# Kernel optimization log

Hardware: AMD Instinct MI355X
Metric: run time of the kernel (lower is better)

Reference implementation:

```python
import jax, jax.numpy as jnp
import numpy as np

HIDDEN = 4096
N_HEADS = 32
N_KV_HEADS = 8
HEAD_DIM = HIDDEN // N_HEADS  # 128
GROUPS = N_HEADS // N_KV_HEADS  # 4
B, S = 1, 2048
NEG = -1e9


def setup_inputs() -> dict:
    key = jax.random.key(0)
    ks = jax.random.split(key, 8)
    hidden_states = jax.random.normal(ks[0], (B, S, HIDDEN), dtype=jnp.float32)
    # additive causal mask [B,1,S,S]
    causal = jnp.tril(jnp.ones((S, S), dtype=bool))
    attention_mask = jnp.where(causal, 0.0, NEG).astype(jnp.float32)[None, None]
    position_ids = jnp.broadcast_to(jnp.arange(S, dtype=jnp.int64), (B, S))
    inv_freq = 1.0 / (500000.0 ** (np.arange(0, HEAD_DIM, 2, dtype=np.float32) / HEAD_DIM))
    freqs = np.arange(S, dtype=np.float32)[:, None] * inv_freq[None, :]  # [S, 64]
    cos = jnp.asarray(np.cos(freqs), dtype=jnp.float32)
    sin = jnp.asarray(np.sin(freqs), dtype=jnp.float32)
    sc = 1.0 / np.sqrt(HIDDEN)
    Wq = jax.random.normal(ks[1], (HIDDEN, HIDDEN), dtype=jnp.float32) * sc
    Wk = jax.random.normal(ks[2], (N_KV_HEADS * HEAD_DIM, HIDDEN), dtype=jnp.float32) * sc
    Wv = jax.random.normal(ks[3], (N_KV_HEADS * HEAD_DIM, HIDDEN), dtype=jnp.float32) * sc
    Wo = jax.random.normal(ks[4], (HIDDEN, HIDDEN), dtype=jnp.float32) * sc
    return {"hidden_states": hidden_states, "attention_mask": attention_mask,
            "position_ids": position_ids, "cos": cos, "sin": sin,
            "Wq": Wq, "Wk": Wk, "Wv": Wv, "Wo": Wo}


def _rope(q, k, cos, sin, position_ids):
    # cos/sin: [max_pos, head_dim//2]; gather per position -> [b,1,s,hd/2]
    c = cos[position_ids][:, None]  # [b,1,s,d/2]
    s_ = sin[position_ids][:, None]
    q1, q2 = q[..., ::2], q[..., 1::2]
    k1, k2 = k[..., ::2], k[..., 1::2]
    q_rot = jnp.concatenate([q1 * c - q2 * s_, q2 * c + q1 * s_], axis=-1)
    k_rot = jnp.concatenate([k1 * c - k2 * s_, k2 * c + k1 * s_], axis=-1)
    return q_rot, k_rot


def reference(hidden_states, attention_mask, position_ids, cos, sin, Wq, Wk, Wv, Wo):
    b, s, _ = hidden_states.shape
    q = jnp.einsum('bsh,oh->bso', hidden_states, Wq).reshape(b, s, N_HEADS, HEAD_DIM).transpose(0, 2, 1, 3)
    k = jnp.einsum('bsh,oh->bso', hidden_states, Wk).reshape(b, s, N_KV_HEADS, HEAD_DIM).transpose(0, 2, 1, 3)
    v = jnp.einsum('bsh,oh->bso', hidden_states, Wv).reshape(b, s, N_KV_HEADS, HEAD_DIM).transpose(0, 2, 1, 3)
    q, k = _rope(q, k, cos, sin, position_ids)
    if GROUPS > 1:
        k = jnp.repeat(k, GROUPS, axis=1)  # [b,H,s,d]
        v = jnp.repeat(v, GROUPS, axis=1)
    scores = jnp.einsum('bhqd,bhkd->bhqk', q, k) / np.sqrt(HEAD_DIM)
    scores = scores + attention_mask
    attn = jax.nn.softmax(scores.astype(jnp.float32), axis=-1).astype(q.dtype)
    out = jnp.einsum('bhqk,bhkd->bhqd', attn, v)
    out = out.transpose(0, 2, 1, 3).reshape(b, s, HIDDEN)
    out = jnp.einsum('bso,ho->bsh', out, Wo)
    return out
```

## Files before the change

### kernel.cpp

```cpp
#include <hip/hip_runtime.h>
#include <hip/hip_bf16.h>

#define S_LEN 2048
#define HID   4096
#define NH    32
#define NKV   8
#define HD    128

typedef __attribute__((ext_vector_type(8))) short short8v;
typedef __attribute__((ext_vector_type(4))) float floatx4;

__device__ __forceinline__ float bf2f(unsigned short u) {
  union { unsigned int u32; float f; } v; v.u32 = ((unsigned int)u) << 16; return v.f;
}
__device__ __forceinline__ unsigned short f2bf(float f) {
  union { float f; unsigned int u; } v; v.f = f;
  unsigned int u = v.u + 0x7fffu + ((v.u >> 16) & 1u);
  return (unsigned short)(u >> 16);
}

__device__ __forceinline__ void gld_lds16(const void* g, void* l) {
  __builtin_amdgcn_global_load_lds((const __attribute__((address_space(1))) void*)g,
                                   (__attribute__((address_space(3))) void*)l, 16, 0, 0);
}

__global__ __launch_bounds__(256) void cvt_all(const float* __restrict__ X,  const float* __restrict__ Wq,
                                               const float* __restrict__ Wk, const float* __restrict__ Wv,
                                               const float* __restrict__ Wo,
                                               unsigned short* __restrict__ Xb,  unsigned short* __restrict__ Wqb,
                                               unsigned short* __restrict__ Wkb, unsigned short* __restrict__ Wvb,
                                               unsigned short* __restrict__ Wob) {
  const int c0 = 2097152;
  const int c1 = c0 + 4194304;
  const int c2 = c1 + 1048576;
  const int c3 = c2 + 1048576;
  const int c4 = c3 + 4194304;
  int i = blockIdx.x * blockDim.x + threadIdx.x;
  int stride = gridDim.x * blockDim.x;
  for (; i < c4; i += stride) {
    const float* src; unsigned short* dst; int off;
    if (i < c0)      { src = X;  dst = Xb;  off = i; }
    else if (i < c1) { src = Wq; dst = Wqb; off = i - c0; }
    else if (i < c2) { src = Wk; dst = Wkb; off = i - c1; }
    else if (i < c3) { src = Wv; dst = Wvb; off = i - c2; }
    else             { src = Wo; dst = Wob; off = i - c3; }
    float4 v = ((const float4*)src)[off];
    ushort4 o;
    o.x = f2bf(v.x); o.y = f2bf(v.y); o.z = f2bf(v.z); o.w = f2bf(v.w);
    ((ushort4*)dst)[off] = o;
  }
}

__device__ __forceinline__ void gemm256_core(const unsigned short* __restrict__ A,
                                             const unsigned short* __restrict__ B,
                                             unsigned short* lds,
                                             int brow, int bcol, int tid,
                                             floatx4 acc[8][4]) {
  const int K = 4096;
  const int w = tid >> 6, lane = tid & 63;
  const int fr = lane & 15, fq = lane >> 4;
  const int wm = w >> 2, wn = w & 3;

  const int r0s = w * 32 + (lane >> 2);
  const int r1s = r0s + 16;
  const int sl0 = ((lane & 3) ^ ((r0s >> 1) & 3)) << 3;
  const int sl1 = ((lane & 3) ^ ((r1s >> 1) & 3)) << 3;
  const unsigned short* pAs0 = A + (size_t)(brow + r0s) * K + sl0;
  const unsigned short* pAs1 = A + (size_t)(brow + r1s) * K + sl1;
  const unsigned short* pBs0 = B + (size_t)(bcol + r0s) * K + sl0;
  const unsigned short* pBs1 = B + (size_t)(bcol + r1s) * K + sl1;

  const int sl = (fq ^ ((fr >> 1) & 3)) << 3;
  int aoffb[8], boffb[4];
#pragma unroll
  for (int m = 0; m < 8; ++m) aoffb[m] = (wm * 128 + m * 16 + fr) * 32 + sl;
#pragma unroll
  for (int n = 0; n < 4; ++n) boffb[n] = 16384 + (wn * 64 + n * 16 + fr) * 32 + sl;

#define STG_A(buf, kh, t)                                                     \
  do {                                                                        \
    const int ko_ = (t) * 64 + (kh) * 32;                                     \
    gld_lds16(pAs0 + ko_, lds + (buf) * 32768 + (kh) * 8192 + w * 1024);      \
    gld_lds16(pAs1 + ko_, lds + (buf) * 32768 + (kh) * 8192 + w * 1024 + 512);\
  } while (0)
#define STG_B(buf, kh, t)                                                     \
  do {                                                                        \
    const int ko_ = (t) * 64 + (kh) * 32;                                     \
    gld_lds16(pBs0 + ko_, lds + (buf) * 32768 + 16384 + (kh) * 8192 + w * 1024);      \
    gld_lds16(pBs1 + ko_, lds + (buf) * 32768 + 16384 + (kh) * 8192 + w * 1024 + 512);\
  } while (0)

  STG_A(0, 0, 0); STG_B(0, 0, 0);
  STG_A(0, 1, 0); STG_B(0, 1, 0);
  STG_A(1, 0, 1); STG_B(1, 0, 1);
  asm volatile("s_waitcnt vmcnt(8)" ::: "memory");
  __builtin_amdgcn_s_barrier();

  const int NT = K / 64;
  for (int t = 0; t < NT; ++t) {
    const int c = t & 1;
    const unsigned short* Lc = lds + c * 32768;
    short8v a_[4], b_[4], a2_[4];

#pragma unroll
    for (int m = 0; m < 4; ++m) a_[m] = *(const short8v*)&Lc[aoffb[m]];
#pragma unroll
    for (int n = 0; n < 4; ++n) b_[n] = *(const short8v*)&Lc[boffb[n]];
    if (t + 1 < NT) STG_A(c ^ 1, 1, t + 1);
    __builtin_amdgcn_s_setprio(1);
#pragma unroll
    for (int m = 0; m < 4; ++m)
#pragma unroll
      for (int n = 0; n < 4; ++n)
        acc[m][n] = __builtin_amdgcn_mfma_f32_16x16x32_bf16(a_[m], b_[n], acc[m][n], 0, 0, 0);
    __builtin_amdgcn_s_setprio(0);
    __builtin_amdgcn_s_barrier();

#pragma unroll
    for (int m = 0; m < 4; ++m) a2_[m] = *(const short8v*)&Lc[aoffb[m + 4]];
    if (t + 1 < NT) STG_B(c ^ 1, 1, t + 1);
    __builtin_amdgcn_s_setprio(1);
#pragma unroll
    for (int m = 0; m < 4; ++m)
#pragma unroll
      for (int n = 0; n < 4; ++n)
        acc[m + 4][n] = __builtin_amdgcn_mfma_f32_16x16x32_bf16(a2_[m], b_[n], acc[m + 4][n], 0, 0, 0);
    __builtin_amdgcn_s_setprio(0);
    if (t == NT - 1) asm volatile("s_waitcnt vmcnt(0)" ::: "memory");
    else             asm volatile("s_waitcnt vmcnt(8)" ::: "memory");
    __builtin_amdgcn_s_barrier();

#pragma unroll
    for (int m = 0; m < 4; ++m) a_[m] = *(const short8v*)&Lc[8192 + aoffb[m]];
#pragma unroll
    for (int n = 0; n < 4; ++n) b_[n] = *(const short8v*)&Lc[8192 + boffb[n]];
    if (t + 2 < NT) STG_A(c, 0, t + 2);
    __builtin_amdgcn_s_setprio(1);
#pragma unroll
    for (int m = 0; m < 4; ++m)
#pragma unroll
      for (int n = 0; n < 4; ++n)
        acc[m][n] = __builtin_amdgcn_mfma_f32_16x16x32_bf16(a_[m], b_[n], acc[m][n], 0, 0, 0);
    __builtin_amdgcn_s_setprio(0);
    __builtin_amdgcn_s_barrier();

#pragma unroll
    for (int m = 0; m < 4; ++m) a2_[m] = *(const short8v*)&Lc[8192 + aoffb[m + 4]];
    if (t + 2 < NT) STG_B(c, 0, t + 2);
    __builtin_amdgcn_s_setprio(1);
#pragma unroll
    for (int m = 0; m < 4; ++m)
#pragma unroll
      for (int n = 0; n < 4; ++n)
        acc[m + 4][n] = __builtin_amdgcn_mfma_f32_16x16x32_bf16(a2_[m], b_[n], acc[m + 4][n], 0, 0, 0);
    __builtin_amdgcn_s_setprio(0);
    if (t >= NT - 2) asm volatile("s_waitcnt vmcnt(0)" ::: "memory");
    else             asm volatile("s_waitcnt vmcnt(8)" ::: "memory");
    __builtin_amdgcn_s_barrier();
  }
#undef STG_A
#undef STG_B
}

__global__ __launch_bounds__(512, 2) void gemm_qkv(const unsigned short* __restrict__ Xb,
                                                   const unsigned short* __restrict__ Wqb,
                                                   const unsigned short* __restrict__ Wkb,
                                                   const unsigned short* __restrict__ Wvb,
                                                   unsigned short* __restrict__ Qg,
                                                   unsigned short* __restrict__ Kg,
                                                   unsigned short* __restrict__ Vt) {
  __shared__ unsigned short lds[2 * 32768];
  const int bx = blockIdx.x;
  const unsigned short* B; unsigned short* C; int mode, bcol, ldc;
  if (bx < 16)      { B = Wqb; C = Qg; mode = 0; bcol = bx * 256;        ldc = HID;  }
  else if (bx < 20) { B = Wkb; C = Kg; mode = 0; bcol = (bx - 16) * 256; ldc = 1024; }
  else              { B = Wvb; C = Vt; mode = 1; bcol = (bx - 20) * 256; ldc = 0;    }
  const int brow = blockIdx.y * 256;
  const int tid = threadIdx.x;
  floatx4 acc[8][4] = {};
  gemm256_core(Xb, B, lds, brow, bcol, tid, acc);

  const int w = tid >> 6, lane = tid & 63;
  const int fr = lane & 15, fq = lane >> 4;
  const int wm = w >> 2, wn = w & 3;
  const int r0 = brow + wm * 128 + fq * 4;
  const int c0 = bcol + wn * 64 + fr;
  if (mode == 0) {
#pragma unroll
    for (int m = 0; m < 8; ++m)
#pragma unroll
      for (int n = 0; n < 4; ++n)
#pragma unroll
        for (int r = 0; r < 4; ++r)
          C[(size_t)(r0 + m * 16 + r) * ldc + c0 + n * 16] = f2bf(acc[m][n][r]);
  } else {
#pragma unroll
    for (int m = 0; m < 8; ++m)
#pragma unroll
      for (int n = 0; n < 4; ++n) {
        ushort4 pk;
        pk.x = f2bf(acc[m][n][0]); pk.y = f2bf(acc[m][n][1]);
        pk.z = f2bf(acc[m][n][2]); pk.w = f2bf(acc[m][n][3]);
        *(ushort4*)&Vt[(size_t)(c0 + n * 16) * S_LEN + (r0 + m * 16)] = pk;
      }
  }
}

__device__ __forceinline__ void gemm_pipe_core(const unsigned short* __restrict__ A,
                                               const unsigned short* __restrict__ B,
                                               unsigned short* lds,
                                               int brow, int bcol, int tid,
                                               floatx4 acc[4][4]) {
  const int K = 4096;
  const int w = tid >> 6, lane = tid & 63;
  const int fr = lane & 15, fq = lane >> 4;
  const int wm = w >> 1, wn = w & 1;

  const int rA0 = tid >> 2, sA = tid & 3;
  const unsigned short* pA0 = A + (size_t)(brow + rA0) * K       + ((sA ^ (rA0 & 3)) << 3);
  const unsigned short* pA1 = A + (size_t)(brow + 128 + rA0) * K + ((sA ^ (rA0 & 3)) << 3);
  const unsigned short* pB0 = B + (size_t)(bcol + rA0) * K       + ((sA ^ (rA0 & 3)) << 3);

  const int sl = (fq ^ (fr & 3)) << 3;
  int aoff[4], boff[4];
#pragma unroll
  for (int m = 0; m < 4; ++m) aoff[m] = (wm * 64 + m * 16 + fr) * 32 + sl;
#pragma unroll
  for (int n = 0; n < 4; ++n) boff[n] = 8192 + (wn * 64 + n * 16 + fr) * 32 + sl;

#define STAGEG(buf, kofs)                                        \
  do {                                                           \
    unsigned short* b_ = lds + (buf) * 12288 + w * 512;          \
    gld_lds16(pA0 + (kofs), b_);                                 \
    gld_lds16(pA1 + (kofs), b_ + 4096);                          \
    gld_lds16(pB0 + (kofs), b_ + 8192);                          \
  } while (0)

  STAGEG(0, 0);
  STAGEG(1, 32);
  asm volatile("s_waitcnt vmcnt(3)" ::: "memory");
  __syncthreads();

  int cb = 0, nb = 2;
  for (int t = 0; t < 128; ++t) {
    if (t + 2 < 128) STAGEG(nb, (t + 2) * 32);

    const unsigned short* Lc = lds + cb * 12288;
    short8v a[4], b[4];
#pragma unroll
    for (int m = 0; m < 4; ++m) a[m] = *(const short8v*)&Lc[aoff[m]];
#pragma unroll
    for (int n = 0; n < 4; ++n) b[n] = *(const short8v*)&Lc[boff[n]];

    __builtin_amdgcn_s_setprio(1);
#pragma unroll
    for (int m = 0; m < 4; ++m)
#pragma unroll
      for (int n = 0; n < 4; ++n)
        acc[m][n] = __builtin_amdgcn_mfma_f32_16x16x32_bf16(a[m], b[n], acc[m][n], 0, 0, 0);
    __builtin_amdgcn_s_setprio(0);

    if (t + 1 < 128) {
      if (t + 2 < 128) asm volatile("s_waitcnt vmcnt(3)" ::: "memory");
      else             asm volatile("s_waitcnt vmcnt(0)" ::: "memory");
      __syncthreads();
      cb = (cb == 2) ? 0 : cb + 1;
      nb = (nb == 2) ? 0 : nb + 1;
    }
  }
#undef STAGEG
}

__global__ __launch_bounds__(512, 4) void gemm_o(const unsigned short* __restrict__ Ao,
                                                 const unsigned short* __restrict__ Wob,
                                                 float* __restrict__ Out) {
  __shared__ unsigned short lds[3 * 12288];
  const int tid = threadIdx.x;
  const int brow = blockIdx.y * 256, bcol = blockIdx.x * 128;
  floatx4 acc[4][4] = {};
  gemm_pipe_core(Ao, Wob, lds, brow, bcol, tid, acc);
  const int w = tid >> 6, lane = tid & 63;
  const int fr = lane & 15, fq = lane >> 4;
  const int r0 = brow + (w >> 1) * 64 + fq * 4;
  const int c0 = bcol + (w & 1) * 64 + fr;
#pragma unroll
  for (int m = 0; m < 4; ++m)
#pragma unroll
    for (int n = 0; n < 4; ++n)
#pragma unroll
      for (int r = 0; r < 4; ++r)
        Out[(size_t)(r0 + m * 16 + r) * HID + c0 + n * 16] = acc[m][n][r];
}

__global__ __launch_bounds__(256) void rope_kernel(const unsigned short* __restrict__ In,
                                                   const float* __restrict__ cosT,
                                                   const float* __restrict__ sinT,
                                                   unsigned short* __restrict__ Out,
                                                   int nh, float scale) {
  int idx = blockIdx.x * 256 + threadIdx.x;
  int j = idx & 63;
  int s = (idx >> 6) & (S_LEN - 1);
  int h = idx >> 17;
  unsigned int pr = *(const unsigned int*)(In + (size_t)s * (nh * HD) + h * HD + 2 * j);
  float q1 = bf2f((unsigned short)(pr & 0xffffu));
  float q2 = bf2f((unsigned short)(pr >> 16));
  float c = cosT[s * 64 + j], sn = sinT[s * 64 + j];
  unsigned short* op = Out + ((size_t)h * S_LEN + s) * HD + j;
  op[0]  = f2bf(scale * (q1 * c - q2 * sn));
  op[64] = f2bf(scale * (q2 * c + q1 * sn));
}

__global__ __launch_bounds__(256) void attn_fwd(const unsigned short* __restrict__ Qr,
                                                const unsigned short* __restrict__ Kr,
                                                const unsigned short* __restrict__ Vt,
                                                unsigned short* __restrict__ Ao) {
  __shared__ unsigned short Kl[2][64 * 128];
  __shared__ unsigned short Vl[2][64 * 128];
  __shared__ unsigned short Pl[4][16 * 72];
  const int id = blockIdx.x;
  const int swz = (id & 7) * 128 + (id >> 3);
  const int h  = swz >> 5;
  const int qt = 31 - (swz & 31);
  const int hk = h >> 2;
  const int qb = qt * 64;
  const int tid = threadIdx.x, w = tid >> 6, lane = tid & 63;
  const int fr = lane & 15, fq = lane >> 4;

  short8v aq[4];
  {
    const unsigned short* qp = Qr + ((size_t)(h * S_LEN + qb + w * 16 + fr)) * HD + fq * 8;
#pragma unroll
    for (int ks = 0; ks < 4; ++ks) aq[ks] = *(const short8v*)(qp + ks * 32);
  }

  const int kcb = ((tid & 15) * 16) ^ (((tid >> 4) & 7) << 4);
  const unsigned short* pK0 = Kr + ((size_t)hk * S_LEN + (tid >> 4)) * HD + (kcb >> 1);
  const int vcb = ((tid & 7) * 16) ^ (((tid >> 3) & 7) << 4);
  const unsigned short* pV0 = Vt + ((size_t)hk * HD + (tid >> 3)) * S_LEN + (vcb >> 1);

  float l_r[4] = {0.f, 0.f, 0.f, 0.f};
  floatx4 o[8] = {};

#define STAGE(buf, t)                                                          \
  do {                                                                         \
    const unsigned short* pk_ = pK0 + (size_t)(t) * 64 * HD;                   \
    const unsigned short* pv_ = pV0 + (t) * 64;                                \
    _Pragma("unroll")                                                          \
    for (int j = 0; j < 4; ++j)                                                \
      gld_lds16(pk_ + (size_t)j * 16 * HD, &Kl[buf][w * 512 + j * 2048]);      \
    _Pragma("unroll")                                                          \
    for (int j = 0; j < 4; ++j)                                                \
      gld_lds16(pv_ + (size_t)j * 32 * S_LEN, &Vl[buf][w * 512 + j * 2048]);   \
  } while (0)

  STAGE(0, 0);
  asm volatile("s_waitcnt vmcnt(0)" ::: "memory");
  __syncthreads();

  int cur = 0;
  for (int t = 0; t <= qt; ++t) {
    const int kv0 = t * 64;
    if (t < qt) STAGE(cur ^ 1, t + 1);

    floatx4 s4[4] = {};
    const unsigned short* Kc = &Kl[cur][0];
    const unsigned short* Vc = &Vl[cur][0];
    __builtin_amdgcn_s_setprio(1);
#pragma unroll
    for (int ks = 0; ks < 4; ++ks) {
#pragma unroll
      for (int n = 0; n < 4; ++n) {
        int row = n * 16 + fr;
        int cb = (ks * 64 + fq * 16) ^ ((row & 7) << 4);
        short8v bk = *(const short8v*)&Kc[row * 128 + (cb >> 1)];
        s4[n] = __builtin_amdgcn_mfma_f32_16x16x32_bf16(aq[ks], bk, s4[n], 0, 0, 0);
      }
    }
    __builtin_amdgcn_s_setprio(0);

    if (t == qt) {
#pragma unroll
      for (int n = 0; n < 4; ++n) {
        int col = kv0 + n * 16 + fr;
#pragma unroll
        for (int r = 0; r < 4; ++r) {
          int rowq = qb + w * 16 + fq * 4 + r;
          if (col > rowq) s4[n][r] = -1e30f;
        }
      }
    }

    float psum[4] = {0.f, 0.f, 0.f, 0.f};
#pragma unroll
    for (int n = 0; n < 4; ++n)
#pragma unroll
      for (int r = 0; r < 4; ++r) {
        float p = exp2f(s4[n][r]);
        psum[r] += p;
        Pl[w][(fq * 4 + r) * 72 + n * 16 + fr] = f2bf(p);
      }
#pragma unroll
    for (int r = 0; r < 4; ++r) l_r[r] += psum[r];

    short8v pa[2];
#pragma unroll
    for (int ks = 0; ks < 2; ++ks)
      pa[ks] = *(const short8v*)&Pl[w][fr * 72 + ks * 32 + fq * 8];
    __builtin_amdgcn_s_setprio(1);
#pragma unroll
    for (int nf = 0; nf < 8; ++nf) {
#pragma unroll
      for (int ks = 0; ks < 2; ++ks) {
        int row = nf * 16 + fr;
        int cb = (ks * 64 + fq * 16) ^ ((row & 7) << 4);
        short8v bv = *(const short8v*)&Vc[row * 64 + (cb >> 1)];
        o[nf] = __builtin_amdgcn_mfma_f32_16x16x32_bf16(pa[ks], bv, o[nf], 0, 0, 0);
      }
    }
    __builtin_amdgcn_s_setprio(0);

    if (t < qt) {
      asm volatile("s_waitcnt vmcnt(0)" ::: "memory");
      __syncthreads();
      cur ^= 1;
    }
  }
#undef STAGE

  float lsum[4];
#pragma unroll
  for (int r = 0; r < 4; ++r) lsum[r] = l_r[r];
#pragma unroll
  for (int off = 8; off; off >>= 1)
#pragma unroll
    for (int r = 0; r < 4; ++r) lsum[r] += __shfl_xor(lsum[r], off);
  float rinv[4];
#pragma unroll
  for (int r = 0; r < 4; ++r) rinv[r] = 1.0f / lsum[r];

  unsigned short* aop = Ao + (size_t)(qb + w * 16 + fq * 4) * HID + h * HD + fr;
#pragma unroll
  for (int nf = 0; nf < 8; ++nf)
#pragma unroll
    for (int r = 0; r < 4; ++r)
      aop[(size_t)r * HID + nf * 16] = f2bf(o[nf][r] * rinv[r]);
}

extern "C" void kernel_launch(void* const* d_in, const int* in_sizes, int n_in,
                              void* d_out, int out_size, void* d_ws, size_t ws_size,
                              hipStream_t stream) {
  (void)in_sizes; (void)n_in; (void)out_size; (void)ws_size;
  const float* X    = (const float*)d_in[0];
  const float* cosT = (const float*)d_in[3];
  const float* sinT = (const float*)d_in[4];
  const float* Wq   = (const float*)d_in[5];
  const float* Wk   = (const float*)d_in[6];
  const float* Wv   = (const float*)d_in[7];
  const float* Wo   = (const float*)d_in[8];

  char* ws = (char*)d_ws;
  size_t off = 0;
  auto alloc = [&](size_t bytes) { char* p = ws + off; off += (bytes + 255) & ~(size_t)255; return p; };
  unsigned short* Xb  = (unsigned short*)alloc((size_t)S_LEN * HID * 2);
  unsigned short* Wqb = (unsigned short*)alloc((size_t)HID * HID * 2);
  unsigned short* Wkb = (unsigned short*)alloc((size_t)1024 * HID * 2);
  unsigned short* Wvb = (unsigned short*)alloc((size_t)1024 * HID * 2);
  unsigned short* Wob = (unsigned short*)alloc((size_t)HID * HID * 2);
  unsigned short* Qg  = (unsigned short*)alloc((size_t)S_LEN * HID * 2);
  unsigned short* Kg  = (unsigned short*)alloc((size_t)S_LEN * 1024 * 2);
  unsigned short* Vt  = (unsigned short*)alloc((size_t)1024 * S_LEN * 2);
  unsigned short* Qr = Wqb;
  unsigned short* Kr = Wqb + (size_t)NH * S_LEN * HD;
  unsigned short* Ao = Xb;

  cvt_all<<<2048, 256, 0, stream>>>(X, Wq, Wk, Wv, Wo, Xb, Wqb, Wkb, Wvb, Wob);
  gemm_qkv<<<dim3(24, 8), 512, 0, stream>>>(Xb, Wqb, Wkb, Wvb, Qg, Kg, Vt);
  rope_kernel<<<(NH * S_LEN * 64) / 256, 256, 0, stream>>>(Qg, cosT, sinT, Qr, NH, 0.12751744f);
  rope_kernel<<<(NKV * S_LEN * 64) / 256, 256, 0, stream>>>(Kg, cosT, sinT, Kr, NKV, 1.0f);
  attn_fwd<<<1024, 256, 0, stream>>>(Qr, Kr, Vt, Ao);
  gemm_o<<<dim3(32, 8), 512, 0, stream>>>(Ao, Wob, (float*)d_out);
}
```

Baseline: 337.4 us.

## Restructure output GEMM pipeline and keep attention P in registers via shuffles

The output-projection GEMM is inlined into its kernel and now loads K-tiles of 64 in two halves, double-buffered with finer-grained vmcnt waits and raw s_barrier. Its LDS swizzle changes and occupancy drops to 2 blocks per CU. The attention kernel computes S transposed (K as the A operand) and packs P to bf16 with v_cvt_pk_bf16_f32. It then builds the PV A-operand with cross-lane shuffles instead of a round trip through LDS, and simplifies the row-sum reduction. The aim is less LDS traffic and fewer barriers, paid for with extra shuffle instructions and lower GEMM occupancy.

```diff
diff --git a/kernel.cpp b/kernel.cpp
--- a/kernel.cpp
+++ b/kernel.cpp
@@ -17,6 +17,11 @@
   union { float f; unsigned int u; } v; v.f = f;
   unsigned int u = v.u + 0x7fffu + ((v.u >> 16) & 1u);
   return (unsigned short)(u >> 16);
+}
+__device__ __forceinline__ unsigned int cvtpk_bf16(float lo, float hi) {
+  unsigned int r;
+  asm("v_cvt_pk_bf16_f32 %0, %1, %2" : "=v"(r) : "v"(lo), "v"(hi));
+  return r;
 }
 
 __device__ __forceinline__ void gld_lds16(const void* g, void* l) {
@@ -206,83 +211,89 @@
   }
 }
 
-__device__ __forceinline__ void gemm_pipe_core(const unsigned short* __restrict__ A,
-                                               const unsigned short* __restrict__ B,
-                                               unsigned short* lds,
-                                               int brow, int bcol, int tid,
-                                               floatx4 acc[4][4]) {
+__global__ __launch_bounds__(512, 2) void gemm_o(const unsigned short* __restrict__ Ao,
+                                                 const unsigned short* __restrict__ Wob,
+                                                 float* __restrict__ Out) {
+  __shared__ unsigned short lds[2 * 24576];
   const int K = 4096;
+  const int tid = threadIdx.x;
   const int w = tid >> 6, lane = tid & 63;
   const int fr = lane & 15, fq = lane >> 4;
   const int wm = w >> 1, wn = w & 1;
-
-  const int rA0 = tid >> 2, sA = tid & 3;
-  const unsigned short* pA0 = A + (size_t)(brow + rA0) * K       + ((sA ^ (rA0 & 3)) << 3);
-  const unsigned short* pA1 = A + (size_t)(brow + 128 + rA0) * K + ((sA ^ (rA0 & 3)) << 3);
-  const unsigned short* pB0 = B + (size_t)(bcol + rA0) * K       + ((sA ^ (rA0 & 3)) << 3);
-
-  const int sl = (fq ^ (fr & 3)) << 3;
+  const int brow = blockIdx.y * 256, bcol = blockIdx.x * 128;
+
+  const int rA = tid >> 2;
+  const int sA = ((tid & 3) ^ ((rA >> 1) & 3)) << 3;
+  const unsigned short* pA0 = Ao  + (size_t)(brow + rA) * K + sA;
+  const unsigned short* pA1 = Ao  + (size_t)(brow + 128 + rA) * K + sA;
+  const unsigned short* pB0 = Wob + (size_t)(bcol + rA) * K + sA;
+
+  const int sl = (fq ^ ((fr >> 1) & 3)) << 3;
   int aoff[4], boff[4];
 #pragma unroll
   for (int m = 0; m < 4; ++m) aoff[m] = (wm * 64 + m * 16 + fr) * 32 + sl;
 #pragma unroll
-  for (int n = 0; n < 4; ++n) boff[n] = 8192 + (wn * 64 + n * 16 + fr) * 32 + sl;
-
-#define STAGEG(buf, kofs)                                        \
-  do {                                                           \
-    unsigned short* b_ = lds + (buf) * 12288 + w * 512;          \
-    gld_lds16(pA0 + (kofs), b_);                                 \
-    gld_lds16(pA1 + (kofs), b_ + 4096);                          \
-    gld_lds16(pB0 + (kofs), b_ + 8192);                          \
+  for (int n = 0; n < 4; ++n) boff[n] = 16384 + (wn * 64 + n * 16 + fr) * 32 + sl;
+
+  floatx4 acc[4][4] = {};
+
+#define STG_KH(buf, kh, t)                                                       \
+  do {                                                                           \
+    const int ko_ = (t) * 64 + (kh) * 32;                                        \
+    gld_lds16(pA0 + ko_, lds + (buf) * 24576 + (kh) * 8192 + w * 512);           \
+    gld_lds16(pA1 + ko_, lds + (buf) * 24576 + (kh) * 8192 + 4096 + w * 512);    \
+    gld_lds16(pB0 + ko_, lds + (buf) * 24576 + 16384 + (kh) * 4096 + w * 512);   \
   } while (0)
 
-  STAGEG(0, 0);
-  STAGEG(1, 32);
-  asm volatile("s_waitcnt vmcnt(3)" ::: "memory");
-  __syncthreads();
-
-  int cb = 0, nb = 2;
-  for (int t = 0; t < 128; ++t) {
-    if (t + 2 < 128) STAGEG(nb, (t + 2) * 32);
-
-    const unsigned short* Lc = lds + cb * 12288;
-    short8v a[4], b[4];
-#pragma unroll
-    for (int m = 0; m < 4; ++m) a[m] = *(const short8v*)&Lc[aoff[m]];
-#pragma unroll
-    for (int n = 0; n < 4; ++n) b[n] = *(const short8v*)&Lc[boff[n]];
-
+  STG_KH(0, 0, 0);
+  STG_KH(0, 1, 0);
+  STG_KH(1, 0, 1);
+  asm volatile("s_waitcnt vmcnt(6)" ::: "memory");
+  __builtin_amdgcn_s_barrier();
+
+  const int NT = K / 64;
+  for (int t = 0; t < NT; ++t) {
+    const int c = t & 1;
+    const unsigned short* Lc = lds + c * 24576;
+    short8v a_[4], b_[4];
+
+#pragma unroll
+    for (int m = 0; m < 4; ++m) a_[m] = *(const short8v*)&Lc[aoff[m]];
+#pragma unroll
+    for (int n = 0; n < 4; ++n) b_[n] = *(const short8v*)&Lc[boff[n]];
+    if (t + 1 < NT) STG_KH(c ^ 1, 1, t + 1);
     __builtin_amdgcn_s_setprio(1);
 #pragma unroll
     for (int m = 0; m < 4; ++m)
 #pragma unroll
       for (int n = 0; n < 4; ++n)
-        acc[m][n] = __builtin_amdgcn_mfma_f32_16x16x32_bf16(a[m], b[n], acc[m][n], 0, 0, 0);
-    __builtin_amdgcn_s_setprio(0);
-
-    if (t + 1 < 128) {
-      if (t + 2 < 128) asm volatile("s_waitcnt vmcnt(3)" ::: "memory");
-      else             asm volatile("s_waitcnt vmcnt(0)" ::: "memory");
-      __syncthreads();
-      cb = (cb == 2) ? 0 : cb + 1;
-      nb = (nb == 2) ? 0 : nb + 1;
-    }
+        acc[m][n] = __builtin_amdgcn_mfma_f32_16x16x32_bf16(a_[m], b_[n], acc[m][n], 0, 0, 0);
+    __builtin_amdgcn_s_setprio(0);
+    if (t + 1 < NT) asm volatile("s_waitcnt vmcnt(6)" ::: "memory");
+    else            asm volatile("s_waitcnt vmcnt(0)" ::: "memory");
+    __builtin_amdgcn_s_barrier();
+
+#pragma unroll
+    for (int m = 0; m < 4; ++m) a_[m] = *(const short8v*)&Lc[8192 + aoff[m]];
+#pragma unroll
+    for (int n = 0; n < 4; ++n) b_[n] = *(const short8v*)&Lc[4096 + boff[n]];
+    if (t + 2 < NT) STG_KH(c, 0, t + 2);
+    __builtin_amdgcn_s_setprio(1);
+#pragma unroll
+    for (int m = 0; m < 4; ++m)
+#pragma unroll
+      for (int n = 0; n < 4; ++n)
+        acc[m][n] = __builtin_amdgcn_mfma_f32_16x16x32_bf16(a_[m], b_[n], acc[m][n], 0, 0, 0);
+    __builtin_amdgcn_s_setprio(0);
+    if (t + 2 < NT)      asm volatile("s_waitcnt vmcnt(6)" ::: "memory");
+    else if (t + 1 < NT) asm volatile("s_waitcnt vmcnt(3)" ::: "memory");
+    else                 asm volatile("s_waitcnt vmcnt(0)" ::: "memory");
+    __builtin_amdgcn_s_barrier();
   }
-#undef STAGEG
-}
-
-__global__ __launch_bounds__(512, 4) void gemm_o(const unsigned short* __restrict__ Ao,
-                                                 const unsigned short* __restrict__ Wob,
-                                                 float* __restrict__ Out) {
-  __shared__ unsigned short lds[3 * 12288];
-  const int tid = threadIdx.x;
-  const int brow = blockIdx.y * 256, bcol = blockIdx.x * 128;
-  floatx4 acc[4][4] = {};
-  gemm_pipe_core(Ao, Wob, lds, brow, bcol, tid, acc);
-  const int w = tid >> 6, lane = tid & 63;
-  const int fr = lane & 15, fq = lane >> 4;
-  const int r0 = brow + (w >> 1) * 64 + fq * 4;
-  const int c0 = bcol + (w & 1) * 64 + fr;
+#undef STG_KH
+
+  const int r0 = brow + wm * 64 + fq * 4;
+  const int c0 = bcol + wn * 64 + fr;
 #pragma unroll
   for (int m = 0; m < 4; ++m)
 #pragma unroll
@@ -316,7 +327,6 @@
                                                 unsigned short* __restrict__ Ao) {
   __shared__ unsigned short Kl[2][64 * 128];
   __shared__ unsigned short Vl[2][64 * 128];
-  __shared__ unsigned short Pl[4][16 * 72];
   const int id = blockIdx.x;
   const int swz = (id & 7) * 128 + (id >> 3);
   const int h  = swz >> 5;
@@ -338,7 +348,11 @@
   const int vcb = ((tid & 7) * 16) ^ (((tid >> 3) & 7) << 4);
   const unsigned short* pV0 = Vt + ((size_t)hk * HD + (tid >> 3)) * S_LEN + (vcb >> 1);
 
-  float l_r[4] = {0.f, 0.f, 0.f, 0.f};
+  const int hsel = fq >> 1;
+  const int srcA = fr + ((2 * (fq & 1)) << 4);
+  const int srcB = fr + ((2 * (fq & 1) + 1) << 4);
+
+  float l_acc = 0.f;
   floatx4 o[8] = {};
 
 #define STAGE(buf, t)                                                          \
@@ -362,7 +376,7 @@
     const int kv0 = t * 64;
     if (t < qt) STAGE(cur ^ 1, t + 1);
 
-    floatx4 s4[4] = {};
+    floatx4 St[4] = {};
     const unsigned short* Kc = &Kl[cur][0];
     const unsigned short* Vc = &Vl[cur][0];
     __builtin_amdgcn_s_setprio(1);
@@ -372,8 +386,8 @@
       for (int n = 0; n < 4; ++n) {
         int row = n * 16 + fr;
         int cb = (ks * 64 + fq * 16) ^ ((row & 7) << 4);
-        short8v bk = *(const short8v*)&Kc[row * 128 + (cb >> 1)];
-        s4[n] = __builtin_amdgcn_mfma_f32_16x16x32_bf16(aq[ks], bk, s4[n], 0, 0, 0);
+        short8v kf = *(const short8v*)&Kc[row * 128 + (cb >> 1)];
+        St[n] = __builtin_amdgcn_mfma_f32_16x16x32_bf16(kf, aq[ks], St[n], 0, 0, 0);
       }
     }
     __builtin_amdgcn_s_setprio(0);
@@ -381,31 +395,41 @@
     if (t == qt) {
 #pragma unroll
       for (int n = 0; n < 4; ++n) {
-        int col = kv0 + n * 16 + fr;
 #pragma unroll
         for (int r = 0; r < 4; ++r) {
-          int rowq = qb + w * 16 + fq * 4 + r;
-          if (col > rowq) s4[n][r] = -1e30f;
+          int kvg = kv0 + n * 16 + fq * 4 + r;
+          if (kvg > qb + w * 16 + fr) St[n][r] = -1e30f;
         }
       }
     }
 
-    float psum[4] = {0.f, 0.f, 0.f, 0.f};
-#pragma unroll
-    for (int n = 0; n < 4; ++n)
-#pragma unroll
-      for (int r = 0; r < 4; ++r) {
-        float p = exp2f(s4[n][r]);
-        psum[r] += p;
-        Pl[w][(fq * 4 + r) * 72 + n * 16 + fr] = f2bf(p);
-      }
-#pragma unroll
-    for (int r = 0; r < 4; ++r) l_r[r] += psum[r];
+    unsigned int pk[4][2];
+#pragma unroll
+    for (int n = 0; n < 4; ++n) {
+      float p0 = exp2f(St[n][0]);
+      float p1 = exp2f(St[n][1]);
+      float p2 = exp2f(St[n][2]);
+      float p3 = exp2f(St[n][3]);
+      l_acc += (p0 + p1) + (p2 + p3);
+      pk[n][0] = cvtpk_bf16(p0, p1);
+      pk[n][1] = cvtpk_bf16(p2, p3);
+    }
 
     short8v pa[2];
 #pragma unroll
-    for (int ks = 0; ks < 2; ++ks)
-      pa[ks] = *(const short8v*)&Pl[w][fr * 72 + ks * 32 + fq * 8];
+    for (int ks = 0; ks < 2; ++ks) {
+      unsigned int v0a = __shfl(pk[2 * ks][0], srcA), v0b = __shfl(pk[2 * ks + 1][0], srcA);
+      unsigned int v1a = __shfl(pk[2 * ks][1], srcA), v1b = __shfl(pk[2 * ks + 1][1], srcA);
+      unsigned int v2a = __shfl(pk[2 * ks][0], srcB), v2b = __shfl(pk[2 * ks + 1][0], srcB);
+      unsigned int v3a = __shfl(pk[2 * ks][1], srcB), v3b = __shfl(pk[2 * ks + 1][1], srcB);
+      uint4 u;
+      u.x = hsel ? v0b : v0a;
+      u.y = hsel ? v1b : v1a;
+      u.z = hsel ? v2b : v2a;
+      u.w = hsel ? v3b : v3a;
+      pa[ks] = *(short8v*)&u;
+    }
+
     __builtin_amdgcn_s_setprio(1);
 #pragma unroll
     for (int nf = 0; nf < 8; ++nf) {
@@ -427,16 +451,12 @@
   }
 #undef STAGE
 
-  float lsum[4];
-#pragma unroll
-  for (int r = 0; r < 4; ++r) lsum[r] = l_r[r];
-#pragma unroll
-  for (int off = 8; off; off >>= 1)
-#pragma unroll
-    for (int r = 0; r < 4; ++r) lsum[r] += __shfl_xor(lsum[r], off);
+  float L = l_acc;
+  L += __shfl_xor(L, 16);
+  L += __shfl_xor(L, 32);
   float rinv[4];
 #pragma unroll
-  for (int r = 0; r < 4; ++r) rinv[r] = 1.0f / lsum[r];
+  for (int r = 0; r < 4; ++r) rinv[r] = 1.0f / __shfl(L, fq * 4 + r);
 
   unsigned short* aop = Ao + (size_t)(qb + w * 16 + fq * 4) * HID + h * HD + fr;
 #pragma unroll
```

New measurement: 323.0 us. 4.3% less time.
